# Kernel tuning notes

Measured on AMD Instinct MI355X. Metric: run time of the kernel, lower is better.

## Reference

```python
import jax, jax.numpy as jnp
import numpy as np

HEADS = 8
DIM_HEAD = 64
WINDOW = 512
SCALE = DIM_HEAD ** -0.5


def setup_inputs() -> dict:
    key = jax.random.key(0)
    k1, k2, k3 = jax.random.split(key, 3)
    b, dim, n = 2, 256, 32768
    hidden = HEADS * DIM_HEAD  # 512
    x = jax.random.normal(k1, (b, dim, n), dtype=jnp.float32)
    # Conv1d(dim, hidden*3, 1, bias=False) weight -> [3*hidden, dim]
    w_qkv = jax.random.normal(k2, (3 * hidden, dim), dtype=jnp.float32) * (dim ** -0.5)
    # Conv1d(hidden, dim, 1) weight/bias
    w_out = jax.random.normal(k3, (dim, hidden), dtype=jnp.float32) * (hidden ** -0.5)
    b_out = jnp.zeros((dim,), dtype=jnp.float32)
    return {"x": x, "w_qkv": w_qkv, "w_out": w_out, "b_out": b_out}


def reference(x, w_qkv, w_out, b_out):
    b, c, n = x.shape
    h, d, w = HEADS, DIM_HEAD, WINDOW
    nw = n // w  # n chosen divisible by window size
    # 1x1 conv == channel matmul
    qkv = jnp.einsum('oc,bcn->bon', w_qkv, x)  # [b, 3*h*d, n]
    q, k, v = jnp.split(qkv, 3, axis=1)
    # [b, h, d, nw, w]
    def to_windows(t):
        return t.reshape(b, h, d, nw, w)
    q = to_windows(q) * SCALE
    k = to_windows(k)
    v = to_windows(v)
    # non-overlapping local windows: block-diagonal attention
    sim = jnp.einsum('bhdni,bhdnj->bhnij', q, k)        # [b,h,nw,w,w]
    attn = jax.nn.softmax(sim, axis=-1)
    out = jnp.einsum('bhnij,bhdnj->bhdni', attn, v)      # [b,h,d,nw,w]
    out = out.reshape(b, h * d, n)
    return jnp.einsum('oc,bcn->bon', w_out, out) + b_out[None, :, None]
```

## Files before the change

### kernel.cpp

```cpp
#include <hip/hip_runtime.h>
#include <stdint.h>
#include <stddef.h>


typedef _Float16 f16;
typedef _Float16 half8 __attribute__((ext_vector_type(8)));
typedef float f32x4 __attribute__((ext_vector_type(4)));

#define NSEQ 32768
#define NTOT 65536
#define WIN  512

__device__ __forceinline__ void async_copy16(const f16* g, f16* l) {
  __builtin_amdgcn_global_load_lds(
      (const __attribute__((address_space(1))) void*)g,
      (__attribute__((address_space(3))) void*)l, 16, 0, 0);
}

__device__ __forceinline__ int packrtz(float a, float b) {
  typedef __fp16 fp16v2 __attribute__((ext_vector_type(2)));
  fp16v2 h = __builtin_amdgcn_cvt_pkrtz(a, b);
  return __builtin_bit_cast(int, h);
}

__global__ __launch_bounds__(256) void convert_w(
    const float* __restrict__ wqkv, const float* __restrict__ wout,
    f16* __restrict__ wqh, f16* __restrict__ woh) {
  int idx = blockIdx.x * 256 + threadIdx.x;
  if (idx < 1536 * 256) {
    float v = wqkv[idx];
    if (idx < 512 * 256) v *= 0.18033688011112042f;
    wqh[idx] = (f16)v;
  } else {
    int j = idx - 1536 * 256;
    if (j < 256 * 512) woh[j] = (f16)wout[j];
  }
}

__global__ __launch_bounds__(256) void transpose_x(
    const float* __restrict__ x, f16* __restrict__ xT) {
  __shared__ alignas(16) float tile[32][33];
  const int tx = threadIdx.x & 31, ty = threadIdx.x >> 5;
  const int bx = blockIdx.x, by = blockIdx.y;
  const float* xb = x + (size_t)blockIdx.z * 256 * NSEQ;
  f16* xTb = xT + (size_t)blockIdx.z * NSEQ * 256;
#pragma unroll
  for (int r = 0; r < 4; ++r) {
    int c = by * 32 + ty + r * 8;
    int n = bx * 32 + tx;
    tile[ty + r * 8][tx] = xb[(size_t)c * NSEQ + n];
  }
  __syncthreads();
  const int tx16 = threadIdx.x & 15, ty16 = threadIdx.x >> 4;
#pragma unroll
  for (int r = 0; r < 2; ++r) {
    int n = bx * 32 + ty16 + r * 16;
    int c = by * 32 + tx16 * 2;
    union {
      f16 h[2];
      int i;
    } u;
    u.h[0] = (f16)tile[tx16 * 2][ty16 + r * 16];
    u.h[1] = (f16)tile[tx16 * 2 + 1][ty16 + r * 16];
    *(int*)(xTb + (size_t)n * 256 + c) = u.i;
  }
}

template <int MODE, int SWZ>
__global__ __launch_bounds__(256) void gemm_k(
    const f16* __restrict__ A, const f16* __restrict__ Bm,
    void* __restrict__ outp, const float* __restrict__ bias, int K,
    int bstride, int ostride) {
  __shared__ alignas(16) f16 As[3][4096];
  __shared__ alignas(16) f16 Bs[3][4096];
  const int tid = threadIdx.x;
  const int lane = tid & 63, wid = tid >> 6;
  const int quad = lane >> 4, lid = lane & 15;

  int colb, rowb;
  if (SWZ) {
    int lin = blockIdx.y * 8 + blockIdx.x;
    int x = lin & 7, s = lin >> 3;
    colb = s & 7;
    rowb = x * 64 + (s >> 3);
  } else {
    colb = blockIdx.x;
    rowb = blockIdx.y;
  }
  const int row0 = rowb * 128, col0 = colb * 128;
  const int wm = (wid >> 1) * 64, wn = (wid & 1) * 64;

  f32x4 acc[4][4];
  const f32x4 zero = {0.f, 0.f, 0.f, 0.f};
#pragma unroll
  for (int i = 0; i < 4; ++i)
#pragma unroll
    for (int j = 0; j < 4; ++j) acc[i][j] = zero;

  const int kIters = K >> 5;

  auto stage = [&](int kt, int buf) {
    const int k0 = kt * 32;
#pragma unroll
    for (int rd = 0; rd < 2; ++rd) {
      int slot = rd * 256 + tid;
      int r = slot & 127, kc = slot >> 7;
      async_copy16(A + (size_t)(row0 + r) * K + k0 + kc * 8,
                   &As[buf][slot * 8]);
      async_copy16(Bm + (size_t)(col0 + r) * bstride + k0 + kc * 8,
                   &Bs[buf][slot * 8]);
    }
  };

  stage(0, 0);
  stage(1, 1);
  for (int kt = 0; kt < kIters; ++kt) {
    const int pb = kt % 3;
    asm volatile("s_waitcnt lgkmcnt(0)" ::: "memory");
    __builtin_amdgcn_sched_barrier(0);
    __builtin_amdgcn_s_barrier();
    __builtin_amdgcn_sched_barrier(0);
    if (kt + 2 < kIters) {
      stage(kt + 2, (kt + 2) % 3);
      asm volatile("s_waitcnt vmcnt(8)" ::: "memory");
    } else if (kt + 1 < kIters) {
      asm volatile("s_waitcnt vmcnt(4)" ::: "memory");
    } else {
      asm volatile("s_waitcnt vmcnt(0)" ::: "memory");
    }
    __builtin_amdgcn_sched_barrier(0);
    __builtin_amdgcn_s_barrier();
    __builtin_amdgcn_sched_barrier(0);

    half8 af[4], bf[4];
#pragma unroll
    for (int mi = 0; mi < 4; ++mi)
      af[mi] = *(const half8*)(&As[pb][(quad * 128 + wm + mi * 16 + lid) * 8]);
#pragma unroll
    for (int ni = 0; ni < 4; ++ni)
      bf[ni] = *(const half8*)(&Bs[pb][(quad * 128 + wn + ni * 16 + lid) * 8]);
#pragma unroll
    for (int mi = 0; mi < 4; ++mi)
#pragma unroll
      for (int ni = 0; ni < 4; ++ni)
        acc[mi][ni] = __builtin_amdgcn_mfma_f32_16x16x32_f16(
            af[mi], bf[ni], acc[mi][ni], 0, 0, 0);
  }

#pragma unroll
  for (int mi = 0; mi < 4; ++mi) {
#pragma unroll
    for (int r = 0; r < 4; ++r) {
      int grow = row0 + wm + mi * 16 + quad * 4 + r;
#pragma unroll
      for (int ni = 0; ni < 4; ++ni) {
        int gcol = col0 + wn + ni * 16 + lid;
        float v = acc[mi][ni][r];
        if (MODE == 2) {
          ((float*)outp)[(size_t)(gcol >> 15) * (256u * 32768u) +
                         (size_t)grow * 32768 + (gcol & 32767)] =
              v + bias[grow];
        } else {
          ((f16*)outp)[(size_t)grow * ostride + gcol] = (f16)v;
        }
      }
    }
  }
}

__global__ __launch_bounds__(512, 2) void attn_k(
    const f16* __restrict__ qk, const f16* __restrict__ vws,
    f16* __restrict__ ows) {
  __shared__ alignas(16) f16 smem[16384];

  const int tid = threadIdx.x;
  const int lane = tid & 63, wid = tid >> 6;
  const int quad = lane >> 4, lid = lane & 15;
  const int win = blockIdx.x;
  const int h = blockIdx.y;
  const size_t nbase = (size_t)blockIdx.z * NSEQ + (size_t)win * WIN;
  const int iw0 = wid * 64;

  half8 aq[4][2];
#pragma unroll
  for (int ig = 0; ig < 4; ++ig)
#pragma unroll
    for (int ks = 0; ks < 2; ++ks)
      aq[ig][ks] = *(const half8*)(qk + (nbase + iw0 + ig * 16 + lid) * 1024 +
                                   h * 64 + ks * 32 + quad * 8);

  f32x4 OT[4][4];
  const f32x4 zero = {0.f, 0.f, 0.f, 0.f};
#pragma unroll
  for (int di = 0; di < 4; ++di)
#pragma unroll
    for (int ig = 0; ig < 4; ++ig) OT[di][ig] = zero;
  float l_run[4] = {0.f, 0.f, 0.f, 0.f};

  const int sa = tid & 63, sc = tid >> 6;
  const int psa = (sa & 32) | ((sa & 12) << 1) | ((sa >> 2) & 4) | (sa & 3);

  async_copy16(qk + (nbase + psa) * 1024 + 512 + h * 64 + sc * 8,
               smem + tid * 8);
  async_copy16(vws + (size_t)(h * 64 + sa) * NTOT + nbase + sc * 8,
               smem + 4096 + tid * 8);

  int p = 0;
  for (int jt = 0; jt < 8; ++jt) {
    __syncthreads();
    if (jt < 7) {
      const int j0n = (jt + 1) * 64;
      f16* Kb = smem + (1 - p) * 8192;
      async_copy16(qk + (nbase + j0n + psa) * 1024 + 512 + h * 64 + sc * 8,
                   Kb + tid * 8);
      async_copy16(vws + (size_t)(h * 64 + sa) * NTOT + nbase + j0n + sc * 8,
                   Kb + 4096 + tid * 8);
    }
    const f16* Ks = smem + p * 8192;
    const f16* Vs = smem + p * 8192 + 4096;

    f32x4 sT[4][4];
#pragma unroll
    for (int jg = 0; jg < 4; ++jg)
#pragma unroll
      for (int ig = 0; ig < 4; ++ig) sT[jg][ig] = zero;
    __builtin_amdgcn_s_setprio(1);
#pragma unroll
    for (int ks = 0; ks < 2; ++ks)
#pragma unroll
      for (int jg = 0; jg < 4; ++jg) {
        half8 bk =
            *(const half8*)(Ks + ((ks * 4 + quad) * 64 + jg * 16 + lid) * 8);
#pragma unroll
        for (int ig = 0; ig < 4; ++ig)
          sT[jg][ig] = __builtin_amdgcn_mfma_f32_16x16x32_f16(
              bk, aq[ig][ks], sT[jg][ig], 0, 0, 0);
      }
    __builtin_amdgcn_s_setprio(0);

    int pk[4][4][2];
#pragma unroll
    for (int jg = 0; jg < 4; ++jg)
#pragma unroll
      for (int ig = 0; ig < 4; ++ig) {
        float e0 = __builtin_amdgcn_exp2f(sT[jg][ig][0]);
        float e1 = __builtin_amdgcn_exp2f(sT[jg][ig][1]);
        float e2 = __builtin_amdgcn_exp2f(sT[jg][ig][2]);
        float e3 = __builtin_amdgcn_exp2f(sT[jg][ig][3]);
        l_run[ig] += (e0 + e1) + (e2 + e3);
        pk[jg][ig][0] = packrtz(e0, e1);
        pk[jg][ig][1] = packrtz(e2, e3);
      }

    __builtin_amdgcn_s_setprio(1);
#pragma unroll
    for (int ks2 = 0; ks2 < 2; ++ks2) {
      const int ta = ks2 * 2, tb = ta + 1;
      half8 pt[4];
#pragma unroll
      for (int ig = 0; ig < 4; ++ig) {
        union {
          int i[4];
          half8 h;
        } u;
        u.i[0] = pk[ta][ig][0];
        u.i[1] = pk[ta][ig][1];
        u.i[2] = pk[tb][ig][0];
        u.i[3] = pk[tb][ig][1];
        pt[ig] = u.h;
      }
#pragma unroll
      for (int di = 0; di < 4; ++di) {
        half8 av =
            *(const half8*)(Vs + ((ks2 * 4 + quad) * 64 + di * 16 + lid) * 8);
#pragma unroll
        for (int ig = 0; ig < 4; ++ig)
          OT[di][ig] = __builtin_amdgcn_mfma_f32_16x16x32_f16(
              av, pt[ig], OT[di][ig], 0, 0, 0);
      }
    }
    __builtin_amdgcn_s_setprio(0);
    p ^= 1;
  }

#pragma unroll
  for (int ig = 0; ig < 4; ++ig) {
    l_run[ig] += __shfl_xor(l_run[ig], 16, 64);
    l_run[ig] += __shfl_xor(l_run[ig], 32, 64);
  }

#pragma unroll
  for (int ig = 0; ig < 4; ++ig) {
    float inv = 1.0f / l_run[ig];
    size_t rowb = (nbase + iw0 + ig * 16 + lid) * 1024 + h * 64;
#pragma unroll
    for (int di = 0; di < 4; ++di) {
      int2 o;
      o.x = packrtz(OT[di][ig][0] * inv, OT[di][ig][1] * inv);
      o.y = packrtz(OT[di][ig][2] * inv, OT[di][ig][3] * inv);
      *(int2*)(ows + rowb + di * 16 + quad * 4) = o;
    }
  }
}

extern "C" void kernel_launch(void* const* d_in, const int* in_sizes, int n_in,
                              void* d_out, int out_size, void* d_ws,
                              size_t ws_size, hipStream_t stream) {
  const float* x = (const float*)d_in[0];
  const float* w_qkv = (const float*)d_in[1];
  const float* w_out = (const float*)d_in[2];
  const float* b_out = (const float*)d_in[3];

  char* ws = (char*)d_ws;
  f16* qkw = (f16*)(ws);
  f16* vw = (f16*)(ws + 134217728);
  f16* xT = (f16*)(ws + 201326592);
  f16* wqh = (f16*)(ws + 234881024);
  f16* woh = (f16*)(ws + 235667456);

  convert_w<<<2048, 256, 0, stream>>>(w_qkv, w_out, wqh, woh);
  transpose_x<<<dim3(1024, 8, 2), 256, 0, stream>>>(x, xT);
  gemm_k<0, 1><<<dim3(8, 512), 256, 0, stream>>>(xT, wqh, qkw, nullptr, 256,
                                                 256, 1024);
  gemm_k<0, 0><<<dim3(512, 4), 256, 0, stream>>>(wqh + 1024 * 256, xT, vw,
                                                 nullptr, 256, 256, NTOT);
  attn_k<<<dim3(64, 8, 2), 512, 0, stream>>>(qkw, vw, qkw);
  gemm_k<2, 0><<<dim3(512, 2), 256, 0, stream>>>(woh, qkw, d_out, b_out, 512,
                                                 1024, 0);
}
```

Before: 384.0 us.

## Triple-buffer K/V tiles in attention kernel with explicit vmcnt waits

Changes the attention kernel's K/V LDS staging from double buffering to a three-deep ring, issuing loads two tiles ahead. Uses explicit s_waitcnt vmcnt counts and paired barriers so each wave waits only for the tile it is about to use. The aim is to hide more global-load latency behind MFMA work. In exchange LDS use grows to 48KB per block, which may limit occupancy at two blocks per CU, and there is one extra barrier per iteration.

```diff
diff --git a/kernel.cpp b/kernel.cpp
--- a/kernel.cpp
+++ b/kernel.cpp
@@ -171,7 +171,7 @@
 __global__ __launch_bounds__(512, 2) void attn_k(
     const f16* __restrict__ qk, const f16* __restrict__ vws,
     f16* __restrict__ ows) {
-  __shared__ alignas(16) f16 smem[16384];
+  __shared__ alignas(16) f16 smem[24576];
 
   const int tid = threadIdx.x;
   const int lane = tid & 63, wid = tid >> 6;
@@ -200,24 +200,38 @@
   const int sa = tid & 63, sc = tid >> 6;
   const int psa = (sa & 32) | ((sa & 12) << 1) | ((sa >> 2) & 4) | (sa & 3);
 
-  async_copy16(qk + (nbase + psa) * 1024 + 512 + h * 64 + sc * 8,
-               smem + tid * 8);
-  async_copy16(vws + (size_t)(h * 64 + sa) * NTOT + nbase + sc * 8,
-               smem + 4096 + tid * 8);
-
-  int p = 0;
+  auto stage = [&](int jt) {
+    f16* Kb = smem + (jt % 3) * 8192;
+    const int j0 = jt * 64;
+    async_copy16(qk + (nbase + j0 + psa) * 1024 + 512 + h * 64 + sc * 8,
+                 Kb + tid * 8);
+    async_copy16(vws + (size_t)(h * 64 + sa) * NTOT + nbase + j0 + sc * 8,
+                 Kb + 4096 + tid * 8);
+  };
+
+  stage(0);
+  stage(1);
+
   for (int jt = 0; jt < 8; ++jt) {
-    __syncthreads();
-    if (jt < 7) {
-      const int j0n = (jt + 1) * 64;
-      f16* Kb = smem + (1 - p) * 8192;
-      async_copy16(qk + (nbase + j0n + psa) * 1024 + 512 + h * 64 + sc * 8,
-                   Kb + tid * 8);
-      async_copy16(vws + (size_t)(h * 64 + sa) * NTOT + nbase + j0n + sc * 8,
-                   Kb + 4096 + tid * 8);
-    }
-    const f16* Ks = smem + p * 8192;
-    const f16* Vs = smem + p * 8192 + 4096;
+    const int pb = jt % 3;
+    asm volatile("s_waitcnt lgkmcnt(0)" ::: "memory");
+    __builtin_amdgcn_sched_barrier(0);
+    __builtin_amdgcn_s_barrier();
+    __builtin_amdgcn_sched_barrier(0);
+    if (jt + 2 < 8) {
+      stage(jt + 2);
+      asm volatile("s_waitcnt vmcnt(4)" ::: "memory");
+    } else if (jt + 1 < 8) {
+      asm volatile("s_waitcnt vmcnt(2)" ::: "memory");
+    } else {
+      asm volatile("s_waitcnt vmcnt(0)" ::: "memory");
+    }
+    __builtin_amdgcn_sched_barrier(0);
+    __builtin_amdgcn_s_barrier();
+    __builtin_amdgcn_sched_barrier(0);
+
+    const f16* Ks = smem + pb * 8192;
+    const f16* Vs = smem + pb * 8192 + 4096;
 
     f32x4 sT[4][4];
 #pragma unroll
@@ -280,7 +294,6 @@
       }
     }
     __builtin_amdgcn_s_setprio(0);
-    p ^= 1;
   }
 
 #pragma unroll
```

Result: slower. 395.3 us (+3.0%).

## Load K and V tiles directly from global memory instead of LDS staging

Applied to the files above, without the earlier changes.

The attention kernel stops staging K and V tiles through double-buffered shared memory with async global-to-LDS copies and block-wide barriers. Each wave now reads its MFMA operands straight from global memory through precomputed per-lane base pointers, relying on L1/L2 caching for reuse across the 8 waves that share the same tiles. This drops the barriers and the LDS footprint, but every wave issues its own global loads with no explicit prefetch, so latency may be exposed and L2 traffic goes up.

```diff
diff --git a/kernel.cpp b/kernel.cpp
--- a/kernel.cpp
+++ b/kernel.cpp
@@ -171,8 +171,6 @@
 __global__ __launch_bounds__(512, 2) void attn_k(
     const f16* __restrict__ qk, const f16* __restrict__ vws,
     f16* __restrict__ ows) {
-  __shared__ alignas(16) f16 smem[16384];
-
   const int tid = threadIdx.x;
   const int lane = tid & 63, wid = tid >> 6;
   const int quad = lane >> 4, lid = lane & 15;
@@ -189,6 +187,20 @@
       aq[ig][ks] = *(const half8*)(qk + (nbase + iw0 + ig * 16 + lid) * 1024 +
                                    h * 64 + ks * 32 + quad * 8);
 
+  const f16* kbase[4];
+#pragma unroll
+  for (int jg = 0; jg < 4; ++jg) {
+    const int pos = jg * 16 + lid;
+    const int prow =
+        (pos & 32) | ((pos & 12) << 1) | ((pos >> 2) & 4) | (pos & 3);
+    kbase[jg] = qk + (nbase + prow) * 1024 + 512 + h * 64 + quad * 8;
+  }
+  const f16* vbase[4];
+#pragma unroll
+  for (int di = 0; di < 4; ++di)
+    vbase[di] =
+        vws + (size_t)(h * 64 + di * 16 + lid) * NTOT + nbase + quad * 8;
+
   f32x4 OT[4][4];
   const f32x4 zero = {0.f, 0.f, 0.f, 0.f};
 #pragma unroll
@@ -197,27 +209,9 @@
     for (int ig = 0; ig < 4; ++ig) OT[di][ig] = zero;
   float l_run[4] = {0.f, 0.f, 0.f, 0.f};
 
-  const int sa = tid & 63, sc = tid >> 6;
-  const int psa = (sa & 32) | ((sa & 12) << 1) | ((sa >> 2) & 4) | (sa & 3);
-
-  async_copy16(qk + (nbase + psa) * 1024 + 512 + h * 64 + sc * 8,
-               smem + tid * 8);
-  async_copy16(vws + (size_t)(h * 64 + sa) * NTOT + nbase + sc * 8,
-               smem + 4096 + tid * 8);
-
-  int p = 0;
+#pragma unroll 1
   for (int jt = 0; jt < 8; ++jt) {
-    __syncthreads();
-    if (jt < 7) {
-      const int j0n = (jt + 1) * 64;
-      f16* Kb = smem + (1 - p) * 8192;
-      async_copy16(qk + (nbase + j0n + psa) * 1024 + 512 + h * 64 + sc * 8,
-                   Kb + tid * 8);
-      async_copy16(vws + (size_t)(h * 64 + sa) * NTOT + nbase + j0n + sc * 8,
-                   Kb + 4096 + tid * 8);
-    }
-    const f16* Ks = smem + p * 8192;
-    const f16* Vs = smem + p * 8192 + 4096;
+    const int jo = jt * 64;
 
     f32x4 sT[4][4];
 #pragma unroll
@@ -229,8 +223,7 @@
     for (int ks = 0; ks < 2; ++ks)
 #pragma unroll
       for (int jg = 0; jg < 4; ++jg) {
-        half8 bk =
-            *(const half8*)(Ks + ((ks * 4 + quad) * 64 + jg * 16 + lid) * 8);
+        half8 bk = *(const half8*)(kbase[jg] + jo * 1024 + ks * 32);
 #pragma unroll
         for (int ig = 0; ig < 4; ++ig)
           sT[jg][ig] = __builtin_amdgcn_mfma_f32_16x16x32_f16(
@@ -271,8 +264,7 @@
       }
 #pragma unroll
       for (int di = 0; di < 4; ++di) {
-        half8 av =
-            *(const half8*)(Vs + ((ks2 * 4 + quad) * 64 + di * 16 + lid) * 8);
+        half8 av = *(const half8*)(vbase[di] + jo + ks2 * 32);
 #pragma unroll
         for (int ig = 0; ig < 4; ++ig)
           OT[di][ig] = __builtin_amdgcn_mfma_f32_16x16x32_f16(
@@ -280,7 +272,6 @@
       }
     }
     __builtin_amdgcn_s_setprio(0);
-    p ^= 1;
   }
 
 #pragma unroll
```

After: 442.6 us. 1.15x slower.
